# Kernel optimization log

Hardware: AMD Instinct MI355X
Metric: run time of the kernel (lower is better)

The kernel has to match this reference:

```python
import jax, jax.numpy as jnp
import numpy as np

N_TRAJ, T, D_DATA, D_LAT, N_UNITS = 8192, 100, 32, 64, 100

def setup_inputs() -> dict:
    key = jax.random.key(0)
    ks = jax.random.split(key, 12)
    w = lambda k, *shape: jax.random.normal(k, shape, jnp.float32) * 0.05
    z = lambda n: jnp.zeros((n,), jnp.float32)
    return {
        "data": jax.random.normal(ks[0], (N_TRAJ, T, D_DATA), jnp.float32),
        "time_steps": jnp.linspace(0.0, 1.0, T, dtype=jnp.float32),  # uniform grid -> dt < interval/50 always
        "prior": jax.random.normal(ks[1], (N_TRAJ, D_LAT), jnp.float32),
        # ODE func MLP: latent -> n_units -> latent
        "Wo1": w(ks[2], D_LAT, N_UNITS), "bo1": z(N_UNITS),
        "Wo2": w(ks[3], N_UNITS, D_LAT), "bo2": z(D_LAT),
        # GRU update/reset/candidate gates, each a 2-layer MLP on concat(y, x)
        "Wz1": w(ks[4], D_LAT + D_DATA, N_UNITS), "bz1": z(N_UNITS),
        "Wz2": w(ks[5], N_UNITS, D_LAT), "bz2": z(D_LAT),
        "Wr1": w(ks[6], D_LAT + D_DATA, N_UNITS), "br1": z(N_UNITS),
        "Wr2": w(ks[7], N_UNITS, D_LAT), "br2": z(D_LAT),
        "Wh1": w(ks[8], D_LAT + D_DATA, N_UNITS), "bh1": z(N_UNITS),
        "Wh2": w(ks[9], N_UNITS, D_LAT), "bh2": z(D_LAT),
    }

def _odernn(data, time_steps, prior,
            Wo1, bo1, Wo2, bo2,
            Wz1, bz1, Wz2, bz2,
            Wr1, br1, Wr2, br2,
            Wh1, bh1, Wh2, bh2):
    # Replicates the original loop's (prev_t, t_i) bookkeeping faithfully:
    # iteration 1 uses dt = ts[1] - ts[0]; after each iteration the code sets
    # prev_t, t_i = ts[i], ts[i-1], so iteration i >= 2 uses dt = ts[i-2] - ts[i-1].
    dts = jnp.concatenate([time_steps[1:2] - time_steps[0:1],
                           time_steps[:-2] - time_steps[1:-1]])  # [T-1]
    xs = jnp.swapaxes(data[:, 1:, :], 0, 1)  # [T-1, N, D_DATA] for scan

    def ode_func(y):  # [N, D_LAT] -> [N, D_LAT]
        return jnp.tanh(y @ Wo1 + bo1) @ Wo2 + bo2

    def gru_update(y, x):  # [N, D_LAT], [N, D_DATA] -> [N, D_LAT]
        yx = jnp.concatenate([y, x], axis=-1)
        zg = jax.nn.sigmoid(jnp.tanh(yx @ Wz1 + bz1) @ Wz2 + bz2)
        rg = jax.nn.sigmoid(jnp.tanh(yx @ Wr1 + br1) @ Wr2 + br2)
        ryx = jnp.concatenate([rg * y, x], axis=-1)
        h = jnp.tanh(jnp.tanh(ryx @ Wh1 + bh1) @ Wh2 + bh2)
        return (1.0 - zg) * h + zg * y

    def step(y, inp):
        dt, x = inp
        # |dt| < minimum_step branch: single explicit-Euler increment
        y_ode = y + ode_func(y) * dt
        return gru_update(y_ode, x), None

    y_final, _ = jax.lax.scan(step, prior, (dts, xs))
    return y_final

def reference(data, time_steps, prior,
              Wo1, bo1, Wo2, bo2,
              Wz1, bz1, Wz2, bz2,
              Wr1, br1, Wr2, br2,
              Wh1, bh1, Wh2, bh2):
    return _odernn(data, time_steps, prior,
                   Wo1, bo1, Wo2, bo2,
                   Wz1, bz1, Wz2, bz2,
                   Wr1, br1, Wr2, br2,
                   Wh1, bh1, Wh2, bh2)
```

## Files before the change

kernel.cpp:

```cpp
#include <hip/hip_runtime.h>

#define T_STEPS 100
#define NTRAJ   8192
#define MBLK    32
#define W_TILES 112
#define W_BYTES (W_TILES * 1024)
#define TILEBUF 18432
#define LDS_TOTAL (W_BYTES + 2 * TILEBUF)

typedef __attribute__((ext_vector_type(8))) _Float16 f16x8;
typedef __attribute__((ext_vector_type(4))) _Float16 f16x4;
typedef __attribute__((ext_vector_type(2))) __fp16   h16x2;
typedef __attribute__((ext_vector_type(4))) float    f32x4;

#define MFMA16(a, b, c) __builtin_amdgcn_mfma_f32_16x16x32_f16((a), (b), (c), 0, 0, 0)

#define SWZ(row, col) ((col) ^ (((row) & 7) << 3))

__device__ __forceinline__ float fast_tanh(float x) {
    float e = __expf(2.f * x);
    return 1.f - 2.f * __builtin_amdgcn_rcpf(1.f + e);
}
__device__ __forceinline__ float fast_sigmoid(float x) {
    float e = __expf(-x);
    return __builtin_amdgcn_rcpf(1.f + e);
}

__global__ void pack_kernel(const float* __restrict__ Wo1, const float* __restrict__ Wo2,
                            const float* __restrict__ Wz1, const float* __restrict__ Wz2,
                            const float* __restrict__ Wr1, const float* __restrict__ Wr2,
                            const float* __restrict__ Wh1, const float* __restrict__ Wh2,
                            _Float16* __restrict__ P)
{
    int idx = blockIdx.x * 256 + threadIdx.x;
    if (idx >= 144 * 512) return;
    int tile = idx >> 9;
    int r    = idx & 511;
    int lane = r >> 3, j = r & 7;
    int krel = ((lane >> 4) << 3) + j;
    int c16  = lane & 15;
    float val = 0.f;

    if (tile < 14) {
        int t = tile, nt = t >> 1, kt = t & 1;
        int k = kt * 32 + krel, n = nt * 16 + c16;
        if (k < 64 && n < 100) val = Wo1[k * 100 + n];
    } else if (tile < 30) {
        int t = tile - 14, nt = t >> 2, kt = t & 3;
        int k = kt * 32 + krel, n = nt * 16 + c16;
        if (k < 100) val = Wo2[k * 64 + n];
    } else if (tile < 75) {
        int t = tile - 30, nt = t / 3, kt = t % 3;
        int k = kt * 32 + krel;
        if (nt < 7)      { int n = nt * 16 + c16;        if (n < 100) val = Wz1[k * 100 + n]; }
        else if (nt >= 8){ int n = (nt - 8) * 16 + c16;  if (n < 100) val = Wr1[k * 100 + n]; }
    } else if (tile < 107) {
        int t = tile - 75, gate = t >> 4, rem = t & 15, nt = rem >> 2, kt = rem & 3;
        int k = kt * 32 + krel, n = nt * 16 + c16;
        const float* W = gate ? Wr2 : Wz2;
        if (k < 100) val = W[k * 64 + n];
    } else if (tile < 128) {
        int t = tile - 107, nt = t / 3, kt = t % 3;
        int k = kt * 32 + krel, n = nt * 16 + c16;
        if (n < 100) val = Wh1[k * 100 + n];
    } else {
        int t = tile - 128, nt = t >> 2, kt = t & 3;
        int k = kt * 32 + krel, n = nt * 16 + c16;
        if (k < 100) val = Wh2[k * 64 + n];
    }
    P[idx] = (_Float16)val;
}

__device__ __forceinline__ f16x8 ldsA(const _Float16* buf, int stride, int row, int kcol) {
    return *(const f16x8*)(buf + row * stride + SWZ(row, kcol));
}
__device__ __forceinline__ void st4(_Float16* buf, int stride, int traj, int f0,
                                    float a, float b, float c, float d) {
    f16x4 h = {(_Float16)a, (_Float16)b, (_Float16)c, (_Float16)d};
    *(f16x4*)(buf + traj * stride + SWZ(traj, f0)) = h;
}
__device__ __forceinline__ f32x4 loadBias4(const float* b, int f0, int n) {
    f32x4 v = {0.f, 0.f, 0.f, 0.f};
    #pragma unroll
    for (int r = 0; r < 4; ++r) if (f0 + r < n) v[r] = b[f0 + r];
    return v;
}
__device__ __forceinline__ f16x8 cvt8(f32x4 a, f32x4 b) {
    union { h16x2 h2[4]; f16x8 v; } u;
    u.h2[0] = __builtin_amdgcn_cvt_pkrtz(a[0], a[1]);
    u.h2[1] = __builtin_amdgcn_cvt_pkrtz(a[2], a[3]);
    u.h2[2] = __builtin_amdgcn_cvt_pkrtz(b[0], b[1]);
    u.h2[3] = __builtin_amdgcn_cvt_pkrtz(b[2], b[3]);
    return u.v;
}

__global__ __launch_bounds__(512, 2) void odernn_kernel(
    const float* __restrict__ data, const float* __restrict__ ts,
    const float* __restrict__ prior,
    const float* __restrict__ bo1, const float* __restrict__ bo2,
    const float* __restrict__ bz1, const float* __restrict__ bz2,
    const float* __restrict__ br1, const float* __restrict__ br2,
    const float* __restrict__ bh1, const float* __restrict__ bh2,
    const _Float16* __restrict__ P, float* __restrict__ out)
{
    extern __shared__ __align__(16) char smem[];
    _Float16* W = (_Float16*)smem;

    const int tid  = threadIdx.x;
    const int lane = tid & 63;
    const int wv   = tid >> 6;
    const int tg   = wv >> 2;
    const int wq   = wv & 3;
    const int c16  = lane & 15;
    const int g4   = lane >> 4;
    const int m0   = blockIdx.x * MBLK + tg * 16;
    const int f0   = wq * 16 + (g4 << 2);
    const f16x8* Pt = (const f16x8*)P;
    const f16x8* Wv = (const f16x8*)W;

    _Float16* base = (_Float16*)(smem + W_BYTES + tg * TILEBUF);
    _Float16* sYb = base;
    _Float16* sYX = base + 1024;
    _Float16* sRX = base + 2048;
    _Float16* sH1 = base + 3072;
    _Float16* sZR = base + 5120;

    {
        f16x8* Wd = (f16x8*)W;
        #pragma unroll
        for (int it = 0; it < 14; ++it) {
            int idx = tid + it * 512;
            int ldst = idx >> 6, l = idx & 63;
            int srct = (ldst < 14) ? ldst : ldst + 16;
            Wd[idx] = Pt[srct * 64 + l];
        }
    }

    int bt3[4];
    #pragma unroll
    for (int q = 0; q < 4; ++q) {
        int i = wq + 4 * q;
        bt3[q] = (i < 14) ? ((i < 7) ? i : i + 1) : 0;
    }
    const int nt1a = wq, nt1b = (wq + 4 < 7) ? wq + 4 : 6;

    f32x4 bo1v[2], bh1v[2], bzrv[4];
    #pragma unroll
    for (int t = 0; t < 2; ++t) {
        int nt = wq + 4 * t;
        f32x4 zo = {0.f,0.f,0.f,0.f};
        if (nt < 7) {
            int ft = nt * 16 + (g4 << 2);
            bo1v[t] = loadBias4(bo1, ft, 100);
            bh1v[t] = loadBias4(bh1, ft, 100);
        } else { bo1v[t] = zo; bh1v[t] = zo; }
    }
    #pragma unroll
    for (int q = 0; q < 4; ++q) {
        int i = wq + 4 * q;
        f32x4 v = {0.f,0.f,0.f,0.f};
        if (i < 14) {
            int ft = bt3[q] * 16 + (g4 << 2);
            if (i < 7) v = loadBias4(bz1, ft, 100);
            else       v = loadBias4(br1, ft - 128, 100);
        }
        bzrv[q] = v;
    }
    const f32x4 bo2v = *(const f32x4*)(bo2 + f0);
    const f32x4 bz2v = *(const f32x4*)(bz2 + f0);
    const f32x4 br2v = *(const f32x4*)(br2 + f0);
    const f32x4 bh2v = *(const f32x4*)(bh2 + f0);

    f16x8 Ao2[4], Ah2[4], Wg4z[4], Wg4r[4], Wg1[2][2], Wx5[2], Wx3[4];
    #pragma unroll
    for (int kt = 0; kt < 4; ++kt) {
        Ao2[kt]  = Pt[(14 + wq * 4 + kt) * 64 + lane];
        Ah2[kt]  = Pt[(128 + wq * 4 + kt) * 64 + lane];
        Wg4z[kt] = Pt[(75 + wq * 4 + kt) * 64 + lane];
        Wg4r[kt] = Pt[(91 + wq * 4 + kt) * 64 + lane];
    }
    #pragma unroll
    for (int kt = 0; kt < 2; ++kt) {
        Wg1[0][kt] = Pt[(nt1a * 2 + kt) * 64 + lane];
        Wg1[1][kt] = Pt[(nt1b * 2 + kt) * 64 + lane];
    }
    Wx5[0] = Pt[(107 + nt1a * 3 + 2) * 64 + lane];
    Wx5[1] = Pt[(107 + nt1b * 3 + 2) * 64 + lane];
    #pragma unroll
    for (int q = 0; q < 4; ++q) Wx3[q] = Pt[(30 + bt3[q] * 3 + 2) * 64 + lane];

    float y[4], yo[4] = {0,0,0,0}, zg[4] = {0,0,0,0};
    {
        f32x4 pv = *(const f32x4*)(prior + (size_t)(m0 + c16) * 64 + f0);
        #pragma unroll
        for (int r = 0; r < 4; ++r) y[r] = pv[r];
        st4(sYb, 64, c16, f0, y[0], y[1], y[2], y[3]);
    }
    {
        int row32 = tid >> 4, col = 112 + (tid & 15);
        int t = row32 >> 4, r16 = row32 & 15;
        _Float16* h1 = (_Float16*)(smem + W_BYTES + t * TILEBUF) + 3072;
        h1[r16 * 128 + SWZ(r16, col)] = (_Float16)0.f;
    }
    for (int i = tid; i < 2 * 16 * 32; i += 512) {
        int t = i >> 9, rem = i & 511;
        int r16 = rem >> 5, cc = rem & 31;
        int col = (cc < 16) ? (112 + cc) : (224 + cc);
        _Float16* zr = (_Float16*)(smem + W_BYTES + t * TILEBUF) + 5120;
        zr[r16 * 256 + SWZ(r16, col)] = (_Float16)0.f;
    }
    __syncthreads();

    const float t0v = ts[0], t1v = ts[1];

    const float* xptr = data + (size_t)(m0 + c16) * (T_STEPS * 32) + 32 + (g4 << 3);
    f32x4 xn0 = *(const f32x4*)(xptr);
    f32x4 xn1 = *(const f32x4*)(xptr + 4);
    f16x8 xfrag = cvt8(xn0, xn1);

    #pragma unroll 1
    for (int s = 0; s < T_STEPS - 1; ++s) {
        const float dt = (s == 0) ? (t1v - t0v) : (ts[s - 1] - ts[s]);

        xptr += 32;
        if (s < T_STEPS - 2) {
            xn0 = *(const f32x4*)(xptr);
            xn1 = *(const f32x4*)(xptr + 4);
        }
        f32x4 xacc3[4];
        {
            f16x8 b0 = ldsA(sYb, 64, c16, (g4 << 3));
            f16x8 b1 = ldsA(sYb, 64, c16, 32 + (g4 << 3));
            #pragma unroll
            for (int q = 0; q < 4; ++q) {
                int i = wq + 4 * q;
                if (i < 14) xacc3[q] = MFMA16(Wx3[q], xfrag, bzrv[q]);
            }
            #pragma unroll
            for (int t = 0; t < 2; ++t) {
                int nt = wq + 4 * t;
                if (nt < 7) {
                    f32x4 acc0 = bo1v[t];
                    f32x4 z4 = {0.f, 0.f, 0.f, 0.f};
                    acc0 = MFMA16(Wg1[t][0], b0, acc0);
                    f32x4 acc1 = MFMA16(Wg1[t][1], b1, z4);
                    int ft = nt * 16 + (g4 << 2);
                    st4(sH1, 128, c16, ft,
                        fast_tanh(acc0[0] + acc1[0]), fast_tanh(acc0[1] + acc1[1]),
                        fast_tanh(acc0[2] + acc1[2]), fast_tanh(acc0[3] + acc1[3]));
                }
            }
        }
        __syncthreads();

        f32x4 xacc5[2];
        {
            f32x4 acc0 = bo2v;
            f32x4 z4 = {0.f, 0.f, 0.f, 0.f};
            acc0 = MFMA16(Ao2[0], ldsA(sH1, 128, c16, 0 * 32 + (g4 << 3)), acc0);
            f32x4 acc1 = MFMA16(Ao2[1], ldsA(sH1, 128, c16, 1 * 32 + (g4 << 3)), z4);
            acc0 = MFMA16(Ao2[2], ldsA(sH1, 128, c16, 2 * 32 + (g4 << 3)), acc0);
            acc1 = MFMA16(Ao2[3], ldsA(sH1, 128, c16, 3 * 32 + (g4 << 3)), acc1);
            #pragma unroll
            for (int t = 0; t < 2; ++t) {
                int nt = wq + 4 * t;
                if (nt < 7) xacc5[t] = MFMA16(Wx5[t], xfrag, bh1v[t]);
            }
            #pragma unroll
            for (int r = 0; r < 4; ++r) yo[r] = y[r] + dt * (acc0[r] + acc1[r]);
            st4(sYX, 64, c16, f0, yo[0], yo[1], yo[2], yo[3]);
        }
        __syncthreads();

        {
            f16x8 b0 = ldsA(sYX, 64, c16, (g4 << 3));
            f16x8 b1 = ldsA(sYX, 64, c16, 32 + (g4 << 3));
            #pragma unroll
            for (int q = 0; q < 4; ++q) {
                int i = wq + 4 * q;
                if (i < 14) {
                    f32x4 acc = MFMA16(Wv[(14 + bt3[q] * 3 + 0) * 64 + lane], b0, xacc3[q]);
                    acc = MFMA16(Wv[(14 + bt3[q] * 3 + 1) * 64 + lane], b1, acc);
                    int ft = bt3[q] * 16 + (g4 << 2);
                    st4(sZR, 256, c16, ft,
                        fast_tanh(acc[0]), fast_tanh(acc[1]),
                        fast_tanh(acc[2]), fast_tanh(acc[3]));
                }
            }
        }
        __syncthreads();

        {
            f32x4 accz0 = bz2v, accr0 = br2v;
            f32x4 z4 = {0.f, 0.f, 0.f, 0.f};
            f32x4 accz1 = z4, accr1 = z4;
            accz0 = MFMA16(Wg4z[0], ldsA(sZR, 256, c16, 0 * 32 + (g4 << 3)), accz0);
            accr0 = MFMA16(Wg4r[0], ldsA(sZR, 256, c16, 128 + 0 * 32 + (g4 << 3)), accr0);
            accz1 = MFMA16(Wg4z[1], ldsA(sZR, 256, c16, 1 * 32 + (g4 << 3)), accz1);
            accr1 = MFMA16(Wg4r[1], ldsA(sZR, 256, c16, 128 + 1 * 32 + (g4 << 3)), accr1);
            accz0 = MFMA16(Wg4z[2], ldsA(sZR, 256, c16, 2 * 32 + (g4 << 3)), accz0);
            accr0 = MFMA16(Wg4r[2], ldsA(sZR, 256, c16, 128 + 2 * 32 + (g4 << 3)), accr0);
            accz1 = MFMA16(Wg4z[3], ldsA(sZR, 256, c16, 3 * 32 + (g4 << 3)), accz1);
            accr1 = MFMA16(Wg4r[3], ldsA(sZR, 256, c16, 128 + 3 * 32 + (g4 << 3)), accr1);
            float rv[4];
            #pragma unroll
            for (int r = 0; r < 4; ++r) {
                zg[r] = fast_sigmoid(accz0[r] + accz1[r]);
                rv[r] = fast_sigmoid(accr0[r] + accr1[r]) * yo[r];
            }
            st4(sRX, 64, c16, f0, rv[0], rv[1], rv[2], rv[3]);
        }
        __syncthreads();

        {
            f16x8 b0 = ldsA(sRX, 64, c16, (g4 << 3));
            f16x8 b1 = ldsA(sRX, 64, c16, 32 + (g4 << 3));
            #pragma unroll
            for (int t = 0; t < 2; ++t) {
                int nt = wq + 4 * t;
                if (nt < 7) {
                    f32x4 acc = MFMA16(Wv[(91 + nt * 3 + 0) * 64 + lane], b0, xacc5[t]);
                    acc = MFMA16(Wv[(91 + nt * 3 + 1) * 64 + lane], b1, acc);
                    int ft = nt * 16 + (g4 << 2);
                    st4(sH1, 128, c16, ft,
                        fast_tanh(acc[0]), fast_tanh(acc[1]),
                        fast_tanh(acc[2]), fast_tanh(acc[3]));
                }
            }
        }
        __syncthreads();

        {
            f32x4 acc0 = bh2v;
            f32x4 z4 = {0.f, 0.f, 0.f, 0.f};
            acc0 = MFMA16(Ah2[0], ldsA(sH1, 128, c16, 0 * 32 + (g4 << 3)), acc0);
            f32x4 acc1 = MFMA16(Ah2[1], ldsA(sH1, 128, c16, 1 * 32 + (g4 << 3)), z4);
            acc0 = MFMA16(Ah2[2], ldsA(sH1, 128, c16, 2 * 32 + (g4 << 3)), acc0);
            acc1 = MFMA16(Ah2[3], ldsA(sH1, 128, c16, 3 * 32 + (g4 << 3)), acc1);
            #pragma unroll
            for (int r = 0; r < 4; ++r) {
                float h = fast_tanh(acc0[r] + acc1[r]);
                y[r] = (1.f - zg[r]) * h + zg[r] * yo[r];
            }
            st4(sYb, 64, c16, f0, y[0], y[1], y[2], y[3]);
        }
        __syncthreads();

        xfrag = cvt8(xn0, xn1);
    }

    {
        f32x4 ov = {y[0], y[1], y[2], y[3]};
        *(f32x4*)(out + (size_t)(m0 + c16) * 64 + f0) = ov;
    }
}

extern "C" void kernel_launch(void* const* d_in, const int* in_sizes, int n_in,
                              void* d_out, int out_size, void* d_ws, size_t ws_size,
                              hipStream_t stream) {
    const float* data = (const float*)d_in[0];
    const float* ts   = (const float*)d_in[1];
    const float* prior= (const float*)d_in[2];
    const float* Wo1 = (const float*)d_in[3];  const float* bo1 = (const float*)d_in[4];
    const float* Wo2 = (const float*)d_in[5];  const float* bo2 = (const float*)d_in[6];
    const float* Wz1 = (const float*)d_in[7];  const float* bz1 = (const float*)d_in[8];
    const float* Wz2 = (const float*)d_in[9];  const float* bz2 = (const float*)d_in[10];
    const float* Wr1 = (const float*)d_in[11]; const float* br1 = (const float*)d_in[12];
    const float* Wr2 = (const float*)d_in[13]; const float* br2 = (const float*)d_in[14];
    const float* Wh1 = (const float*)d_in[15]; const float* bh1 = (const float*)d_in[16];
    const float* Wh2 = (const float*)d_in[17]; const float* bh2 = (const float*)d_in[18];
    _Float16* P = (_Float16*)d_ws;
    float* out = (float*)d_out;

    (void)hipFuncSetAttribute((const void*)odernn_kernel,
                              hipFuncAttributeMaxDynamicSharedMemorySize, LDS_TOTAL);

    hipLaunchKernelGGL(pack_kernel, dim3((144 * 512 + 255) / 256), dim3(256), 0, stream,
                       Wo1, Wo2, Wz1, Wz2, Wr1, Wr2, Wh1, Wh2, P);
    hipLaunchKernelGGL(odernn_kernel, dim3(NTRAJ / MBLK), dim3(512), LDS_TOTAL, stream,
                       data, ts, prior, bo1, bo2, bz1, bz2, br1, br2, bh1, bh2, P, out);
}
```

Measured before the change: 268.8 us.

## Halve block size to one trajectory group and shrink LDS weight cache

Each block now processes 16 trajectories with 4 waves instead of 32 with 8. The LDS weight cache keeps only the y-part tiles of the gate and candidate first layers, repacked contiguously. This cuts LDS use so more independent blocks can share a CU and barriers span fewer waves. The cost is that each block reloads its own copy of the weights, and the launch now relies on the default LDS limit instead of setting the attribute.

```diff
diff --git a/kernel.cpp b/kernel.cpp
--- a/kernel.cpp
+++ b/kernel.cpp
@@ -2,11 +2,11 @@
 
 #define T_STEPS 100
 #define NTRAJ   8192
-#define MBLK    32
-#define W_TILES 112
+#define MBLK    16
+#define W_TILES 44
 #define W_BYTES (W_TILES * 1024)
 #define TILEBUF 18432
-#define LDS_TOTAL (W_BYTES + 2 * TILEBUF)
+#define LDS_TOTAL (W_BYTES + TILEBUF)
 
 typedef __attribute__((ext_vector_type(8))) _Float16 f16x8;
 typedef __attribute__((ext_vector_type(4))) _Float16 f16x4;
@@ -94,7 +94,7 @@
     return u.v;
 }
 
-__global__ __launch_bounds__(512, 2) void odernn_kernel(
+__global__ __launch_bounds__(256, 2) void odernn_kernel(
     const float* __restrict__ data, const float* __restrict__ ts,
     const float* __restrict__ prior,
     const float* __restrict__ bo1, const float* __restrict__ bo2,
@@ -108,17 +108,15 @@
 
     const int tid  = threadIdx.x;
     const int lane = tid & 63;
-    const int wv   = tid >> 6;
-    const int tg   = wv >> 2;
-    const int wq   = wv & 3;
+    const int wq   = tid >> 6;
     const int c16  = lane & 15;
     const int g4   = lane >> 4;
-    const int m0   = blockIdx.x * MBLK + tg * 16;
+    const int m0   = blockIdx.x * MBLK;
     const int f0   = wq * 16 + (g4 << 2);
     const f16x8* Pt = (const f16x8*)P;
     const f16x8* Wv = (const f16x8*)W;
 
-    _Float16* base = (_Float16*)(smem + W_BYTES + tg * TILEBUF);
+    _Float16* base = (_Float16*)(smem + W_BYTES);
     _Float16* sYb = base;
     _Float16* sYX = base + 1024;
     _Float16* sRX = base + 2048;
@@ -127,12 +125,11 @@
 
     {
         f16x8* Wd = (f16x8*)W;
-        #pragma unroll
-        for (int it = 0; it < 14; ++it) {
-            int idx = tid + it * 512;
-            int ldst = idx >> 6, l = idx & 63;
-            int srct = (ldst < 14) ? ldst : ldst + 16;
-            Wd[idx] = Pt[srct * 64 + l];
+        for (int idx = tid; idx < W_TILES * 64; idx += 256) {
+            int c = idx >> 6, l = idx & 63;
+            int src = (c < 30) ? (30 + (c >> 1) * 3 + (c & 1))
+                               : (107 + ((c - 30) >> 1) * 3 + ((c - 30) & 1));
+            Wd[idx] = Pt[src * 64 + l];
         }
     }
 
@@ -197,17 +194,13 @@
         st4(sYb, 64, c16, f0, y[0], y[1], y[2], y[3]);
     }
     {
-        int row32 = tid >> 4, col = 112 + (tid & 15);
-        int t = row32 >> 4, r16 = row32 & 15;
-        _Float16* h1 = (_Float16*)(smem + W_BYTES + t * TILEBUF) + 3072;
-        h1[r16 * 128 + SWZ(r16, col)] = (_Float16)0.f;
-    }
-    for (int i = tid; i < 2 * 16 * 32; i += 512) {
-        int t = i >> 9, rem = i & 511;
-        int r16 = rem >> 5, cc = rem & 31;
+        int row = tid >> 4, col = 112 + (tid & 15);
+        sH1[row * 128 + SWZ(row, col)] = (_Float16)0.f;
+    }
+    for (int i = tid; i < 16 * 32; i += 256) {
+        int r16 = i >> 5, cc = i & 31;
         int col = (cc < 16) ? (112 + cc) : (224 + cc);
-        _Float16* zr = (_Float16*)(smem + W_BYTES + t * TILEBUF) + 5120;
-        zr[r16 * 256 + SWZ(r16, col)] = (_Float16)0.f;
+        sZR[r16 * 256 + SWZ(r16, col)] = (_Float16)0.f;
     }
     __syncthreads();
 
@@ -279,8 +272,8 @@
             for (int q = 0; q < 4; ++q) {
                 int i = wq + 4 * q;
                 if (i < 14) {
-                    f32x4 acc = MFMA16(Wv[(14 + bt3[q] * 3 + 0) * 64 + lane], b0, xacc3[q]);
-                    acc = MFMA16(Wv[(14 + bt3[q] * 3 + 1) * 64 + lane], b1, acc);
+                    f32x4 acc = MFMA16(Wv[(bt3[q] * 2 + 0) * 64 + lane], b0, xacc3[q]);
+                    acc = MFMA16(Wv[(bt3[q] * 2 + 1) * 64 + lane], b1, acc);
                     int ft = bt3[q] * 16 + (g4 << 2);
                     st4(sZR, 256, c16, ft,
                         fast_tanh(acc[0]), fast_tanh(acc[1]),
@@ -319,8 +312,8 @@
             for (int t = 0; t < 2; ++t) {
                 int nt = wq + 4 * t;
                 if (nt < 7) {
-                    f32x4 acc = MFMA16(Wv[(91 + nt * 3 + 0) * 64 + lane], b0, xacc5[t]);
-                    acc = MFMA16(Wv[(91 + nt * 3 + 1) * 64 + lane], b1, acc);
+                    f32x4 acc = MFMA16(Wv[(30 + nt * 2 + 0) * 64 + lane], b0, xacc5[t]);
+                    acc = MFMA16(Wv[(30 + nt * 2 + 1) * 64 + lane], b1, acc);
                     int ft = nt * 16 + (g4 << 2);
                     st4(sH1, 128, c16, ft,
                         fast_tanh(acc[0]), fast_tanh(acc[1]),
@@ -372,11 +365,8 @@
     _Float16* P = (_Float16*)d_ws;
     float* out = (float*)d_out;
 
-    (void)hipFuncSetAttribute((const void*)odernn_kernel,
-                              hipFuncAttributeMaxDynamicSharedMemorySize, LDS_TOTAL);
-
     hipLaunchKernelGGL(pack_kernel, dim3((144 * 512 + 255) / 256), dim3(256), 0, stream,
                        Wo1, Wo2, Wz1, Wz2, Wr1, Wr2, Wh1, Wh2, P);
-    hipLaunchKernelGGL(odernn_kernel, dim3(NTRAJ / MBLK), dim3(512), LDS_TOTAL, stream,
+    hipLaunchKernelGGL(odernn_kernel, dim3(NTRAJ / MBLK), dim3(256), LDS_TOTAL, stream,
                        data, ts, prior, bo1, bo2, bz1, bz2, br1, br2, bh1, bh2, P, out);
 }
```

New measurement: 265.1 us, median of 2. About the same (-1.4%).
